# Kernel tuning notes

Measured on AMD Instinct MI355X. Metric: run time of the kernel, lower is better.

Reference implementation:

```python
import jax, jax.numpy as jnp
import numpy as np

LATENT = 512
RNN = 512
CODE = 512
INP = 2
MIX = 5
BATCH = 4096
SEGMENTS = 512


def _p(key, shape, scale=0.05):
    return jax.random.normal(key, shape, dtype=jnp.float32) * scale


def setup_inputs() -> dict:
    key = jax.random.key(0)
    ks = jax.random.split(key, 20)
    return {
        "latent": jax.random.normal(ks[0], (BATCH, LATENT), dtype=jnp.float32),
        "W_unpack": _p(ks[1], (CODE, LATENT)),
        "b_unpack": _p(ks[2], (CODE,)),
        "W_ih1": _p(ks[3], (4 * RNN, CODE + INP)),
        "W_hh1": _p(ks[4], (4 * RNN, RNN)),
        "b_ih1": _p(ks[5], (4 * RNN,)),
        "b_hh1": _p(ks[6], (4 * RNN,)),
        "W_ih2": _p(ks[7], (4 * RNN, RNN)),
        "W_hh2": _p(ks[8], (4 * RNN, RNN)),
        "b_ih2": _p(ks[9], (4 * RNN,)),
        "b_hh2": _p(ks[10], (4 * RNN,)),
        "W_mu": _p(ks[11], (MIX, RNN)),
        "b_mu": _p(ks[12], (MIX,)),
        "W_var": _p(ks[13], (MIX, RNN)),
        "b_var": _p(ks[14], (MIX,)),
        "W_mix": _p(ks[15], (MIX, RNN)),
        "b_mix": _p(ks[16], (MIX,)),
        "eps": jax.random.normal(ks[17], (SEGMENTS, BATCH, 1), dtype=jnp.float32),
        "num_segments": SEGMENTS,
    }


def _lstm_cell(x, h, c, W_ih, W_hh, b_ih, b_hh):
    # PyTorch LSTMCell: gate order i, f, g, o
    gates = x @ W_ih.T + b_ih + h @ W_hh.T + b_hh
    i, f, g, o = jnp.split(gates, 4, axis=-1)
    c_new = jax.nn.sigmoid(f) * c + jax.nn.sigmoid(i) * jnp.tanh(g)
    h_new = jax.nn.sigmoid(o) * jnp.tanh(c_new)
    return h_new, c_new


def reference(latent, W_unpack, b_unpack, W_ih1, W_hh1, b_ih1, b_hh1,
              W_ih2, W_hh2, b_ih2, b_hh2, W_mu, b_mu, W_var, b_var,
              W_mix, b_mix, eps, num_segments):
    t = 0.0  # default temperature arg
    B = latent.shape[0]
    idea = jnp.tanh(latent @ W_unpack.T + b_unpack)  # [B, CODE]

    def step(carry, eps_s):
        prev, h1, c1, h2, c2 = carry
        x = jnp.concatenate([idea, prev], axis=-1)          # [B, CODE+2]
        h1, c1 = _lstm_cell(x, h1, c1, W_ih1, W_hh1, b_ih1, b_hh1)
        h2, c2 = _lstm_cell(h1, h2, c2, W_ih2, W_hh2, b_ih2, b_hh2)
        rho = jax.nn.softmax(h2 @ W_mix.T + b_mix, axis=-1)  # [B, MIX]
        mu = jnp.sum(rho * (h2 @ W_mu.T + b_mu), axis=-1, keepdims=True)
        sigma = jnp.sum(rho * jnp.exp(h2 @ W_var.T + b_var - t), axis=-1, keepdims=True)
        angles = jnp.tanh(mu + sigma * eps_s)                # rsample + tanh, [B, 1]
        prev = jnp.concatenate([angles, jnp.zeros_like(angles)], axis=-1)
        return (prev, h1, c1, h2, c2), angles

    z = jnp.zeros((B, RNN), dtype=latent.dtype)
    carry0 = (jnp.zeros((B, INP), dtype=latent.dtype), z, z, z, z)
    _, angles = jax.lax.scan(step, carry0, eps)              # [S, B, 1]
    level = jnp.concatenate([angles, jnp.zeros_like(angles)], axis=-1)  # [S, B, 2]
    return jnp.transpose(level, (1, 0, 2))                   # [B, S, 2]
```

## Files before the change

kernel.cpp:

```cpp
#include <hip/hip_runtime.h>
#include <stdint.h>

#define BATCH 4096
#define RNN   512
#define SEGS  512

typedef __attribute__((ext_vector_type(8))) short bf16x8;
typedef __attribute__((ext_vector_type(4))) float f32x4;

#define MODE_TANH  0
#define MODE_BASE  1
#define MODE_CELL1 2
#define MODE_CELL2 3

#define GLD_LDS16(g, l) \
  __builtin_amdgcn_global_load_lds((const __attribute__((address_space(1))) void*)(g), \
                                   (__attribute__((address_space(3))) void*)(l), 16, 0, 0)

__device__ __forceinline__ unsigned short f2bf(float f){
  unsigned u = __float_as_uint(f);
  u += 0x7FFF + ((u >> 16) & 1);
  return (unsigned short)(u >> 16);
}
__device__ __forceinline__ float bf2f(unsigned short s){
  return __uint_as_float(((unsigned)s) << 16);
}
__device__ __forceinline__ float fsigmoid(float x){ return 1.0f / (1.0f + __expf(-x)); }
__device__ __forceinline__ float ftanh(float x){
  float e = __expf(-2.0f * fabsf(x));
  float t = (1.0f - e) / (1.0f + e);
  return copysignf(t, x);
}


__global__ void prep_cvt(const float* __restrict__ x, short* __restrict__ y, int n){
  int i = blockIdx.x * 256 + threadIdx.x;
  if (i < n) y[i] = (short)f2bf(x[i]);
}

__global__ void prep_reorder(
    const float* __restrict__ W_ih1, const float* __restrict__ W_hh1,
    const float* __restrict__ b_ih1, const float* __restrict__ b_hh1,
    const float* __restrict__ W_ih2, const float* __restrict__ W_hh2,
    const float* __restrict__ b_ih2, const float* __restrict__ b_hh2,
    short* __restrict__ Wr1, short* __restrict__ W1c,
    short* __restrict__ Wr2i, short* __restrict__ Wr2h,
    float* __restrict__ w1r, float* __restrict__ b1r, float* __restrict__ b2r)
{
  int idx = blockIdx.x * 256 + threadIdx.x;
  if (idx >= 2048 * 512) return;
  int rn = idx >> 9;
  int k  = idx & 511;
  int j = rn >> 2, g = rn & 3;
  int ro = g * 512 + j;
  Wr1 [idx] = (short)f2bf(W_hh1[(size_t)ro * 512 + k]);
  W1c [idx] = (short)f2bf(W_ih1[(size_t)ro * 514 + k]);
  Wr2i[idx] = (short)f2bf(W_ih2[(size_t)ro * 512 + k]);
  Wr2h[idx] = (short)f2bf(W_hh2[(size_t)ro * 512 + k]);
  if (k == 0){
    w1r[rn] = W_ih1[(size_t)ro * 514 + 512];
    b1r[rn] = b_ih1[ro] + b_hh1[ro];
    b2r[rn] = b_ih2[ro] + b_hh2[ro];
  }
}

__global__ void prep_whead(const float* __restrict__ Wmu, const float* __restrict__ Wvar,
                           const float* __restrict__ Wmix, short* __restrict__ Wh){
  int i = blockIdx.x * 256 + threadIdx.x;
  if (i >= 16 * 512) return;
  int n = i >> 9, k = i & 511;
  float v = (n < 5) ? Wmu[n * 512 + k] : (n < 10) ? Wvar[(n - 5) * 512 + k]
          : (n < 15) ? Wmix[(n - 10) * 512 + k] : 0.f;
  Wh[i] = (short)f2bf(v);
}

__global__ __launch_bounds__(256) void gemm_fused(
    const short* __restrict__ A1, const short* __restrict__ B1,
    const short* __restrict__ A2, const short* __restrict__ B2,
    int k1, int k2, int N, int mode,
    const float* __restrict__ bias,
    const unsigned short* __restrict__ base1,
    const float* __restrict__ w1r,
    float* __restrict__ cbuf,
    void* __restrict__ outp,
    const short* __restrict__ h2prev, const short* __restrict__ Whead,
    const float* __restrict__ bmu, const float* __restrict__ bvar,
    const float* __restrict__ bmix, const float* __restrict__ eps,
    float* __restrict__ fout, int s)
{
  __shared__ __align__(16) short As[8192];
  __shared__ __align__(16) short Bs[8192];
  __shared__ __align__(16) float headP[128 * 16];
  __shared__ float angS[128];

  const int tid  = threadIdx.x;
  const int lane = tid & 63;
  const int wave = tid >> 6;
  const int wm = wave >> 1, wn = wave & 1;
  const int m0 = blockIdx.y * 128, n0 = blockIdx.x * 128;

  int aoff[4], boff[4];
  #pragma unroll
  for (int j = 0; j < 4; j++){
    int c = (wave * 4 + j) * 64 + lane;
    int quad = c & 3, r16 = (c >> 2) & 15, kw = (c >> 6) & 1, g = c >> 7;
    int row = g * 16 + r16, col = kw * 32 + quad * 8;
    aoff[j] = (m0 + row) * 512 + col;
    boff[j] = (n0 + row) * 512 + col;
  }

  f32x4 acc[4][4];
  #pragma unroll
  for (int i = 0; i < 4; i++)
    #pragma unroll
    for (int j = 0; j < 4; j++)
      acc[i][j] = (f32x4){0.f, 0.f, 0.f, 0.f};

  const int nk = (k1 + k2) >> 6;

  auto stage = [&](int it){
    int ko = it << 6;
    const short* Ap; const short* Bp; int kk;
    if (ko < k1){ Ap = A1; Bp = B1; kk = ko; }
    else        { Ap = A2; Bp = B2; kk = ko - k1; }
    #pragma unroll
    for (int j = 0; j < 4; j++){
      GLD_LDS16(Ap + aoff[j] + kk, (char*)As + (wave * 4 + j) * 1024);
      GLD_LDS16(Bp + boff[j] + kk, (char*)Bs + (wave * 4 + j) * 1024);
    }
  };

  const int fro = ((lane & 15) * 4 + (lane >> 4)) * 8;

  auto compute = [&](){
    #pragma unroll
    for (int kw = 0; kw < 2; ++kw){
      bf16x8 af[4], bfr[4];
      #pragma unroll
      for (int f = 0; f < 4; f++){
        af[f]  = *(const bf16x8*)&As[((wm * 4 + f) * 2 + kw) * 512 + fro];
        bfr[f] = *(const bf16x8*)&Bs[((wn * 4 + f) * 2 + kw) * 512 + fro];
      }
      #pragma unroll
      for (int mf = 0; mf < 4; mf++)
        #pragma unroll
        for (int nf = 0; nf < 4; nf++)
          acc[mf][nf] = __builtin_amdgcn_mfma_f32_16x16x32_bf16(af[mf], bfr[nf], acc[mf][nf], 0, 0, 0);
    }
  };

  stage(0);

  if (mode == MODE_CELL1 && s > 0){
    const int g0 = wave * 2;
    f32x4 pa0 = {0.f,0.f,0.f,0.f}, pa1 = {0.f,0.f,0.f,0.f};
    const int arow = m0 + g0 * 16 + (lane & 15);
    const int koff = (lane >> 4) * 8;
    #pragma unroll
    for (int k0 = 0; k0 < 512; k0 += 32){
      bf16x8 bfh = *(const bf16x8*)&Whead[(lane & 15) * 512 + k0 + koff];
      bf16x8 a0  = *(const bf16x8*)&h2prev[(size_t)arow * 512 + k0 + koff];
      bf16x8 a1  = *(const bf16x8*)&h2prev[(size_t)(arow + 16) * 512 + k0 + koff];
      pa0 = __builtin_amdgcn_mfma_f32_16x16x32_bf16(a0, bfh, pa0, 0, 0, 0);
      pa1 = __builtin_amdgcn_mfma_f32_16x16x32_bf16(a1, bfh, pa1, 0, 0, 0);
    }
    #pragma unroll
    for (int r = 0; r < 4; r++){
      headP[((g0    ) * 16 + (lane >> 4) * 4 + r) * 16 + (lane & 15)] = pa0[r];
      headP[((g0 + 1) * 16 + (lane >> 4) * 4 + r) * 16 + (lane & 15)] = pa1[r];
    }
  }

  __syncthreads();

  if (mode == MODE_CELL1){
    if (s > 0){
      if (tid < 128){
        float p[15];
        #pragma unroll
        for (int k = 0; k < 15; k++) p[k] = headP[tid * 16 + k];
        float l[5], mx = -1e30f;
        #pragma unroll
        for (int k = 0; k < 5; k++){ l[k] = p[10 + k] + bmix[k]; mx = fmaxf(mx, l[k]); }
        float se = 0.f, e[5];
        #pragma unroll
        for (int k = 0; k < 5; k++){ e[k] = __expf(l[k] - mx); se += e[k]; }
        float inv = 1.0f / se, mu = 0.f, sg = 0.f;
        #pragma unroll
        for (int k = 0; k < 5; k++){
          float rho = e[k] * inv;
          mu += rho * (p[k] + bmu[k]);
          sg += rho * __expf(p[5 + k] + bvar[k]);
        }
        float a = ftanh(mu + sg * eps[(size_t)(s - 1) * BATCH + m0 + tid]);
        angS[tid] = a;
        if (blockIdx.x == 0){
          size_t o = ((size_t)(m0 + tid) * SEGS + (s - 1)) * 2;
          fout[o] = a; fout[o + 1] = 0.0f;
        }
      }
    } else if (tid < 128) angS[tid] = 0.f;
  }

  compute();
  __syncthreads();

  for (int it = 1; it < nk; ++it){
    stage(it);
    __syncthreads();
    compute();
    __syncthreads();
  }

  const int lr = (lane >> 4) * 4;
  const int lc = lane & 15;

  if (mode == MODE_TANH){
    unsigned short* out = (unsigned short*)outp;
    #pragma unroll
    for (int mf = 0; mf < 4; mf++)
      #pragma unroll
      for (int nf = 0; nf < 4; nf++)
        #pragma unroll
        for (int r = 0; r < 4; r++){
          int grow = m0 + wm * 64 + mf * 16 + lr + r;
          int gcol = n0 + wn * 64 + nf * 16 + lc;
          float v = acc[mf][nf][r] + bias[gcol];
          out[(size_t)grow * N + gcol] = f2bf(ftanh(v));
        }
  } else if (mode == MODE_BASE){
    unsigned short* out = (unsigned short*)outp;
    #pragma unroll
    for (int mf = 0; mf < 4; mf++)
      #pragma unroll
      for (int nf = 0; nf < 4; nf++)
        #pragma unroll
        for (int r = 0; r < 4; r++){
          int grow = m0 + wm * 64 + mf * 16 + lr + r;
          int gcol = n0 + wn * 64 + nf * 16 + lc;
          out[(size_t)grow * N + gcol] = f2bf(acc[mf][nf][r] + bias[gcol]);
        }
  } else {
    unsigned short* hout = (unsigned short*)outp;
    const int q = lane & 3;
    #pragma unroll
    for (int mf = 0; mf < 4; mf++)
      #pragma unroll
      for (int nf = 0; nf < 4; nf++)
        #pragma unroll
        for (int r = 0; r < 4; r++){
          int grow = m0 + wm * 64 + mf * 16 + lr + r;
          int gcol = n0 + wn * 64 + nf * 16 + lc;
          float v = acc[mf][nf][r];
          if (mode == MODE_CELL1)
            v += bf2f(base1[(size_t)grow * 2048 + gcol]) + angS[grow - m0] * w1r[gcol];
          else
            v += bias[gcol];
          float x1 = __shfl_xor(v, 1);
          float x2 = __shfl_xor(v, 2);
          float x3 = __shfl_xor(v, 3);
          if (q == 0){
            int j = gcol >> 2;
            size_t ci = (size_t)grow * 512 + j;
            float co = cbuf[ci];
            float cn = fsigmoid(x1) * co + fsigmoid(v) * ftanh(x2);
            float hn = fsigmoid(x3) * ftanh(cn);
            cbuf[ci] = cn;
            hout[ci] = f2bf(hn);
          }
        }
  }
}

__global__ __launch_bounds__(256) void head_step(
    const short* __restrict__ h2,
    const float* __restrict__ Wmu,  const float* __restrict__ bmu,
    const float* __restrict__ Wvar, const float* __restrict__ bvar,
    const float* __restrict__ Wmix, const float* __restrict__ bmix,
    const float* __restrict__ eps,  float* __restrict__ ang,
    float* __restrict__ out, int s)
{
  const int lane = threadIdx.x & 63;
  const int wave = threadIdx.x >> 6;
  const int row = blockIdx.x * 4 + wave;

  uint4 hv = *(const uint4*)&h2[(size_t)row * 512 + lane * 8];
  const unsigned short* hs = (const unsigned short*)&hv;
  float h[8];
  #pragma unroll
  for (int j = 0; j < 8; j++) h[j] = bf2f(hs[j]);

  float p[15];
  #pragma unroll
  for (int k = 0; k < 5; k++){
    const float4* wm4 = (const float4*)(Wmu  + (size_t)k * 512 + lane * 8);
    const float4* wv4 = (const float4*)(Wvar + (size_t)k * 512 + lane * 8);
    const float4* wx4 = (const float4*)(Wmix + (size_t)k * 512 + lane * 8);
    float4 a0 = wm4[0], a1 = wm4[1];
    float4 v0 = wv4[0], v1 = wv4[1];
    float4 x0 = wx4[0], x1 = wx4[1];
    p[k]      = h[0]*a0.x + h[1]*a0.y + h[2]*a0.z + h[3]*a0.w + h[4]*a1.x + h[5]*a1.y + h[6]*a1.z + h[7]*a1.w;
    p[5 + k]  = h[0]*v0.x + h[1]*v0.y + h[2]*v0.z + h[3]*v0.w + h[4]*v1.x + h[5]*v1.y + h[6]*v1.z + h[7]*v1.w;
    p[10 + k] = h[0]*x0.x + h[1]*x0.y + h[2]*x0.z + h[3]*x0.w + h[4]*x1.x + h[5]*x1.y + h[6]*x1.z + h[7]*x1.w;
  }
  #pragma unroll
  for (int k = 0; k < 15; k++){
    #pragma unroll
    for (int off = 1; off < 64; off <<= 1)
      p[k] += __shfl_xor(p[k], off);
  }
  if (lane == 0){
    float l[5], mx = -1e30f;
    #pragma unroll
    for (int k = 0; k < 5; k++){ l[k] = p[10 + k] + bmix[k]; mx = fmaxf(mx, l[k]); }
    float se = 0.f, e[5];
    #pragma unroll
    for (int k = 0; k < 5; k++){ e[k] = __expf(l[k] - mx); se += e[k]; }
    float inv = 1.0f / se, mu = 0.f, sg = 0.f;
    #pragma unroll
    for (int k = 0; k < 5; k++){
      float rho = e[k] * inv;
      mu += rho * (p[k] + bmu[k]);
      sg += rho * __expf(p[5 + k] + bvar[k]);
    }
    float a = ftanh(mu + sg * eps[(size_t)s * BATCH + row]);
    ang[row] = a;
    size_t o = ((size_t)row * SEGS + s) * 2;
    out[o]     = a;
    out[o + 1] = 0.0f;
  }
}


extern "C" void kernel_launch(void* const* d_in, const int* in_sizes, int n_in,
                              void* d_out, int out_size, void* d_ws, size_t ws_size,
                              hipStream_t stream)
{
  const float* latent   = (const float*)d_in[0];
  const float* W_unpack = (const float*)d_in[1];
  const float* b_unpack = (const float*)d_in[2];
  const float* W_ih1    = (const float*)d_in[3];
  const float* W_hh1    = (const float*)d_in[4];
  const float* b_ih1    = (const float*)d_in[5];
  const float* b_hh1    = (const float*)d_in[6];
  const float* W_ih2    = (const float*)d_in[7];
  const float* W_hh2    = (const float*)d_in[8];
  const float* b_ih2    = (const float*)d_in[9];
  const float* b_hh2    = (const float*)d_in[10];
  const float* W_mu     = (const float*)d_in[11];
  const float* b_mu     = (const float*)d_in[12];
  const float* W_var    = (const float*)d_in[13];
  const float* b_var    = (const float*)d_in[14];
  const float* W_mix    = (const float*)d_in[15];
  const float* b_mix    = (const float*)d_in[16];
  const float* eps      = (const float*)d_in[17];
  float* out = (float*)d_out;

  char* p = (char*)d_ws;
  auto alloc = [&](size_t b) -> void* {
    void* r = (void*)p;
    p += (b + 255) & ~(size_t)255;
    return r;
  };
  short* latb  = (short*)alloc((size_t)BATCH * 512 * 2);
  short* Wub   = (short*)alloc((size_t)512 * 512 * 2);
  short* idea  = (short*)alloc((size_t)BATCH * 512 * 2);
  unsigned short* base1 = (unsigned short*)alloc((size_t)BATCH * 2048 * 2);
  short* Wr1   = (short*)alloc((size_t)2048 * 512 * 2);
  short* W1c   = (short*)alloc((size_t)2048 * 512 * 2);
  short* Wr2i  = (short*)alloc((size_t)2048 * 512 * 2);
  short* Wr2h  = (short*)alloc((size_t)2048 * 512 * 2);
  short* Whead = (short*)alloc((size_t)16 * 512 * 2);
  float* w1r   = (float*)alloc(2048 * 4);
  float* b1r   = (float*)alloc(2048 * 4);
  float* b2r   = (float*)alloc(2048 * 4);
  short* h1a   = (short*)alloc((size_t)BATCH * 512 * 2);
  short* h1b   = (short*)alloc((size_t)BATCH * 512 * 2);
  short* h2a   = (short*)alloc((size_t)BATCH * 512 * 2);
  short* h2b   = (short*)alloc((size_t)BATCH * 512 * 2);
  float* c1    = (float*)alloc((size_t)BATCH * 512 * 4);
  float* c2    = (float*)alloc((size_t)BATCH * 512 * 4);
  float* ang   = (float*)alloc(BATCH * 4);
  short* h1[2] = {h1a, h1b};
  short* h2[2] = {h2a, h2b};

  hipMemsetAsync(h1[0], 0, (size_t)BATCH * 512 * 2, stream);
  hipMemsetAsync(h2[0], 0, (size_t)BATCH * 512 * 2, stream);
  hipMemsetAsync(c1, 0, (size_t)BATCH * 512 * 4, stream);
  hipMemsetAsync(c2, 0, (size_t)BATCH * 512 * 4, stream);

  prep_cvt<<<(BATCH * 512) / 256, 256, 0, stream>>>(latent, latb, BATCH * 512);
  prep_cvt<<<(512 * 512) / 256, 256, 0, stream>>>(W_unpack, Wub, 512 * 512);
  prep_reorder<<<(2048 * 512) / 256, 256, 0, stream>>>(
      W_ih1, W_hh1, b_ih1, b_hh1, W_ih2, W_hh2, b_ih2, b_hh2,
      Wr1, W1c, Wr2i, Wr2h, w1r, b1r, b2r);
  prep_whead<<<32, 256, 0, stream>>>(W_mu, W_var, W_mix, Whead);

  dim3 blk(256);
  gemm_fused<<<dim3(4, 32), blk, 0, stream>>>(
      latb, Wub, nullptr, nullptr, 512, 0, 512, MODE_TANH,
      b_unpack, nullptr, nullptr, nullptr, (void*)idea,
      nullptr, nullptr, nullptr, nullptr, nullptr, nullptr, nullptr, 0);
  gemm_fused<<<dim3(16, 32), blk, 0, stream>>>(
      idea, W1c, nullptr, nullptr, 512, 0, 2048, MODE_BASE,
      b1r, nullptr, nullptr, nullptr, (void*)base1,
      nullptr, nullptr, nullptr, nullptr, nullptr, nullptr, nullptr, 0);

  int cur = 0;
  for (int s = 0; s < SEGS; ++s){
    gemm_fused<<<dim3(16, 32), blk, 0, stream>>>(
        h1[cur], Wr1, nullptr, nullptr, 512, 0, 2048, MODE_CELL1,
        nullptr, base1, w1r, c1, (void*)h1[cur ^ 1],
        h2[cur], Whead, b_mu, b_var, b_mix, eps, out, s);
    gemm_fused<<<dim3(16, 32), blk, 0, stream>>>(
        h1[cur ^ 1], Wr2i, h2[cur], Wr2h, 512, 512, 2048, MODE_CELL2,
        b2r, nullptr, nullptr, c2, (void*)h2[cur ^ 1],
        nullptr, nullptr, nullptr, nullptr, nullptr, nullptr, nullptr, 0);
    cur ^= 1;
  }
  head_step<<<BATCH / 4, 256, 0, stream>>>(
      h2[cur], W_mu, b_mu, W_var, b_var, W_mix, b_mix, eps, ang, out, SEGS - 1);
}
```

Baseline: 61.10 ms.

## Replace per-step kernel launches with a persistent grid-synchronized LSTM scan kernel

Moves the 512-step recurrence from 1024 separate kernel launches into one persistent kernel that loops over steps and tiles. Phases are separated by an atomic-counter grid barrier, with the grid size taken from the occupancy query. This removes launch overhead and the gaps between dependent launches, at the cost of spin-wait barrier latency. The barrier relies on all blocks being co-resident and has a timeout bail-out that could silently break ordering.

```diff
diff --git a/kernel.cpp b/kernel.cpp
--- a/kernel.cpp
+++ b/kernel.cpp
@@ -90,8 +90,6 @@
 {
   __shared__ __align__(16) short As[8192];
   __shared__ __align__(16) short Bs[8192];
-  __shared__ __align__(16) float headP[128 * 16];
-  __shared__ float angS[128];
 
   const int tid  = threadIdx.x;
   const int lane = tid & 63;
@@ -150,8 +148,140 @@
   };
 
   stage(0);
-
-  if (mode == MODE_CELL1 && s > 0){
+  __syncthreads();
+  compute();
+  __syncthreads();
+  for (int it = 1; it < nk; ++it){
+    stage(it);
+    __syncthreads();
+    compute();
+    __syncthreads();
+  }
+
+  const int lr = (lane >> 4) * 4;
+  const int lc = lane & 15;
+
+  if (mode == MODE_TANH){
+    unsigned short* out = (unsigned short*)outp;
+    #pragma unroll
+    for (int mf = 0; mf < 4; mf++)
+      #pragma unroll
+      for (int nf = 0; nf < 4; nf++)
+        #pragma unroll
+        for (int r = 0; r < 4; r++){
+          int grow = m0 + wm * 64 + mf * 16 + lr + r;
+          int gcol = n0 + wn * 64 + nf * 16 + lc;
+          float v = acc[mf][nf][r] + bias[gcol];
+          out[(size_t)grow * N + gcol] = f2bf(ftanh(v));
+        }
+  } else {
+    unsigned short* out = (unsigned short*)outp;
+    #pragma unroll
+    for (int mf = 0; mf < 4; mf++)
+      #pragma unroll
+      for (int nf = 0; nf < 4; nf++)
+        #pragma unroll
+        for (int r = 0; r < 4; r++){
+          int grow = m0 + wm * 64 + mf * 16 + lr + r;
+          int gcol = n0 + wn * 64 + nf * 16 + lc;
+          out[(size_t)grow * N + gcol] = f2bf(acc[mf][nf][r] + bias[gcol]);
+        }
+  }
+}
+
+__device__ __forceinline__ void gridbar(unsigned* cnt, int G, int& gen, bool& bail){
+  __syncthreads();
+  if (threadIdx.x == 0){
+    gen++;
+    __threadfence();
+    __hip_atomic_fetch_add(cnt, 1u, __ATOMIC_RELAXED, __HIP_MEMORY_SCOPE_AGENT);
+    if (!bail){
+      const unsigned tgt = (unsigned)G * (unsigned)gen;
+      unsigned iters = 0;
+      while (__hip_atomic_load(cnt, __ATOMIC_RELAXED, __HIP_MEMORY_SCOPE_AGENT) < tgt){
+        __builtin_amdgcn_s_sleep(2);
+        if (++iters > (1u << 24)) { bail = true; break; }
+      }
+    }
+    __threadfence();
+  }
+  __syncthreads();
+}
+
+template<int PHASE>
+__device__ __forceinline__ void run_tile(
+    int t, int s,
+    const short* __restrict__ A1, const short* __restrict__ B1,
+    const short* __restrict__ A2, const short* __restrict__ B2,
+    const unsigned short* __restrict__ base1, const float* __restrict__ w1r,
+    const float* __restrict__ bias2,
+    float* __restrict__ cbuf, unsigned short* __restrict__ hout,
+    const short* __restrict__ h2prev, const short* __restrict__ Whead,
+    const float* __restrict__ bmu, const float* __restrict__ bvar,
+    const float* __restrict__ bmix, const float* __restrict__ eps,
+    float* __restrict__ fout,
+    short* As, short* Bs, float* headP, float* angS)
+{
+  const int tid  = threadIdx.x;
+  const int lane = tid & 63;
+  const int wave = tid >> 6;
+  const int wm = wave >> 1, wn = wave & 1;
+  const int bx = t & 15, by = t >> 4;
+  const int m0 = by * 128, n0 = bx * 128;
+
+  int aoff[4], boff[4];
+  #pragma unroll
+  for (int j = 0; j < 4; j++){
+    int c = (wave * 4 + j) * 64 + lane;
+    int quad = c & 3, r16 = (c >> 2) & 15, kw = (c >> 6) & 1, g = c >> 7;
+    int row = g * 16 + r16, col = kw * 32 + quad * 8;
+    aoff[j] = (m0 + row) * 512 + col;
+    boff[j] = (n0 + row) * 512 + col;
+  }
+
+  f32x4 acc[4][4];
+  #pragma unroll
+  for (int i = 0; i < 4; i++)
+    #pragma unroll
+    for (int j = 0; j < 4; j++)
+      acc[i][j] = (f32x4){0.f, 0.f, 0.f, 0.f};
+
+  const int nk = (PHASE == 1) ? 8 : 16;
+
+  auto stage = [&](int it){
+    int ko = it << 6;
+    const short* Ap; const short* Bp; int kk;
+    if (PHASE == 1 || ko < 512){ Ap = A1; Bp = B1; kk = ko; }
+    else                       { Ap = A2; Bp = B2; kk = ko - 512; }
+    #pragma unroll
+    for (int j = 0; j < 4; j++){
+      GLD_LDS16(Ap + aoff[j] + kk, (char*)As + (wave * 4 + j) * 1024);
+      GLD_LDS16(Bp + boff[j] + kk, (char*)Bs + (wave * 4 + j) * 1024);
+    }
+  };
+
+  const int fro = ((lane & 15) * 4 + (lane >> 4)) * 8;
+
+  auto compute = [&](){
+    #pragma unroll
+    for (int kw = 0; kw < 2; ++kw){
+      bf16x8 af[4], bfr[4];
+      #pragma unroll
+      for (int f = 0; f < 4; f++){
+        af[f]  = *(const bf16x8*)&As[((wm * 4 + f) * 2 + kw) * 512 + fro];
+        bfr[f] = *(const bf16x8*)&Bs[((wn * 4 + f) * 2 + kw) * 512 + fro];
+      }
+      #pragma unroll
+      for (int mf = 0; mf < 4; mf++)
+        #pragma unroll
+        for (int nf = 0; nf < 4; nf++)
+          acc[mf][nf] = __builtin_amdgcn_mfma_f32_16x16x32_bf16(af[mf], bfr[nf], acc[mf][nf], 0, 0, 0);
+    }
+  };
+
+  stage(0);
+
+  if (PHASE == 1 && s > 0){
     const int g0 = wave * 2;
     f32x4 pa0 = {0.f,0.f,0.f,0.f}, pa1 = {0.f,0.f,0.f,0.f};
     const int arow = m0 + g0 * 16 + (lane & 15);
@@ -173,7 +303,7 @@
 
   __syncthreads();
 
-  if (mode == MODE_CELL1){
+  if (PHASE == 1){
     if (s > 0){
       if (tid < 128){
         float p[15];
@@ -194,7 +324,7 @@
         }
         float a = ftanh(mu + sg * eps[(size_t)(s - 1) * BATCH + m0 + tid]);
         angS[tid] = a;
-        if (blockIdx.x == 0){
+        if (bx == 0){
           size_t o = ((size_t)(m0 + tid) * SEGS + (s - 1)) * 2;
           fout[o] = a; fout[o + 1] = 0.0f;
         }
@@ -214,61 +344,74 @@
 
   const int lr = (lane >> 4) * 4;
   const int lc = lane & 15;
-
-  if (mode == MODE_TANH){
-    unsigned short* out = (unsigned short*)outp;
-    #pragma unroll
-    for (int mf = 0; mf < 4; mf++)
-      #pragma unroll
-      for (int nf = 0; nf < 4; nf++)
-        #pragma unroll
-        for (int r = 0; r < 4; r++){
-          int grow = m0 + wm * 64 + mf * 16 + lr + r;
-          int gcol = n0 + wn * 64 + nf * 16 + lc;
-          float v = acc[mf][nf][r] + bias[gcol];
-          out[(size_t)grow * N + gcol] = f2bf(ftanh(v));
+  const int q = lane & 3;
+  #pragma unroll
+  for (int mf = 0; mf < 4; mf++)
+    #pragma unroll
+    for (int nf = 0; nf < 4; nf++)
+      #pragma unroll
+      for (int r = 0; r < 4; r++){
+        int grow = m0 + wm * 64 + mf * 16 + lr + r;
+        int gcol = n0 + wn * 64 + nf * 16 + lc;
+        float v = acc[mf][nf][r];
+        if (PHASE == 1)
+          v += bf2f(base1[(size_t)grow * 2048 + gcol]) + angS[grow - m0] * w1r[gcol];
+        else
+          v += bias2[gcol];
+        float x1 = __shfl_xor(v, 1);
+        float x2 = __shfl_xor(v, 2);
+        float x3 = __shfl_xor(v, 3);
+        if (q == 0){
+          int j = gcol >> 2;
+          size_t ci = (size_t)grow * 512 + j;
+          float co = cbuf[ci];
+          float cn = fsigmoid(x1) * co + fsigmoid(v) * ftanh(x2);
+          float hn = fsigmoid(x3) * ftanh(cn);
+          cbuf[ci] = cn;
+          hout[ci] = f2bf(hn);
         }
-  } else if (mode == MODE_BASE){
-    unsigned short* out = (unsigned short*)outp;
-    #pragma unroll
-    for (int mf = 0; mf < 4; mf++)
-      #pragma unroll
-      for (int nf = 0; nf < 4; nf++)
-        #pragma unroll
-        for (int r = 0; r < 4; r++){
-          int grow = m0 + wm * 64 + mf * 16 + lr + r;
-          int gcol = n0 + wn * 64 + nf * 16 + lc;
-          out[(size_t)grow * N + gcol] = f2bf(acc[mf][nf][r] + bias[gcol]);
-        }
-  } else {
-    unsigned short* hout = (unsigned short*)outp;
-    const int q = lane & 3;
-    #pragma unroll
-    for (int mf = 0; mf < 4; mf++)
-      #pragma unroll
-      for (int nf = 0; nf < 4; nf++)
-        #pragma unroll
-        for (int r = 0; r < 4; r++){
-          int grow = m0 + wm * 64 + mf * 16 + lr + r;
-          int gcol = n0 + wn * 64 + nf * 16 + lc;
-          float v = acc[mf][nf][r];
-          if (mode == MODE_CELL1)
-            v += bf2f(base1[(size_t)grow * 2048 + gcol]) + angS[grow - m0] * w1r[gcol];
-          else
-            v += bias[gcol];
-          float x1 = __shfl_xor(v, 1);
-          float x2 = __shfl_xor(v, 2);
-          float x3 = __shfl_xor(v, 3);
-          if (q == 0){
-            int j = gcol >> 2;
-            size_t ci = (size_t)grow * 512 + j;
-            float co = cbuf[ci];
-            float cn = fsigmoid(x1) * co + fsigmoid(v) * ftanh(x2);
-            float hn = fsigmoid(x3) * ftanh(cn);
-            cbuf[ci] = cn;
-            hout[ci] = f2bf(hn);
-          }
-        }
+      }
+}
+
+__global__ __launch_bounds__(256) void lstm_scan(
+    const short* __restrict__ Wr1, const short* __restrict__ Wr2i, const short* __restrict__ Wr2h,
+    const unsigned short* __restrict__ base1,
+    const float* __restrict__ w1r, const float* __restrict__ b2r,
+    float* __restrict__ c1, float* __restrict__ c2,
+    short* __restrict__ h1A, short* __restrict__ h1B,
+    short* __restrict__ h2A, short* __restrict__ h2B,
+    const short* __restrict__ Whead,
+    const float* __restrict__ bmu, const float* __restrict__ bvar, const float* __restrict__ bmix,
+    const float* __restrict__ eps, float* __restrict__ fout,
+    unsigned* __restrict__ barcnt)
+{
+  __shared__ __align__(16) short As[8192];
+  __shared__ __align__(16) short Bs[8192];
+  __shared__ __align__(16) float headP[128 * 16];
+  __shared__ float angS[128];
+
+  const int bid = blockIdx.x;
+  const int G   = gridDim.x;
+  int gen = 0;
+  bool bail = false;
+
+  for (int s = 0; s < SEGS; ++s){
+    const short* h1in  = (s & 1) ? h1B : h1A;
+    short*       h1out = (s & 1) ? h1A : h1B;
+    const short* h2in  = (s & 1) ? h2B : h2A;
+    short*       h2out = (s & 1) ? h2A : h2B;
+
+    for (int t = bid; t < 512; t += G)
+      run_tile<1>(t, s, h1in, Wr1, nullptr, nullptr, base1, w1r, nullptr,
+                  c1, (unsigned short*)h1out, h2in, Whead, bmu, bvar, bmix,
+                  eps, fout, As, Bs, headP, angS);
+    gridbar(barcnt, G, gen, bail);
+
+    for (int t = bid; t < 512; t += G)
+      run_tile<2>(t, s, h1out, Wr2i, h2in, Wr2h, nullptr, nullptr, b2r,
+                  c2, (unsigned short*)h2out, nullptr, nullptr, nullptr, nullptr,
+                  nullptr, nullptr, fout, As, Bs, headP, angS);
+    gridbar(barcnt, G, gen, bail);
   }
 }
 
@@ -381,13 +524,26 @@
   float* c1    = (float*)alloc((size_t)BATCH * 512 * 4);
   float* c2    = (float*)alloc((size_t)BATCH * 512 * 4);
   float* ang   = (float*)alloc(BATCH * 4);
-  short* h1[2] = {h1a, h1b};
-  short* h2[2] = {h2a, h2b};
-
-  hipMemsetAsync(h1[0], 0, (size_t)BATCH * 512 * 2, stream);
-  hipMemsetAsync(h2[0], 0, (size_t)BATCH * 512 * 2, stream);
+  unsigned* barcnt = (unsigned*)alloc(256);
+
+  static int g_G = 0;
+  if (g_G == 0){
+    int occ = 0, ncu = 256, dev = 0;
+    if (hipOccupancyMaxActiveBlocksPerMultiprocessor(&occ, lstm_scan, 256, 0) != hipSuccess || occ < 1)
+      occ = 1;
+    hipDeviceProp_t prop;
+    if (hipGetDevice(&dev) == hipSuccess && hipGetDeviceProperties(&prop, dev) == hipSuccess)
+      ncu = prop.multiProcessorCount;
+    long g = (long)occ * (long)ncu;
+    g_G = (g > 512) ? 512 : (int)g;
+    if (g_G < 1) g_G = 256;
+  }
+
+  hipMemsetAsync(h1a, 0, (size_t)BATCH * 512 * 2, stream);
+  hipMemsetAsync(h2a, 0, (size_t)BATCH * 512 * 2, stream);
   hipMemsetAsync(c1, 0, (size_t)BATCH * 512 * 4, stream);
   hipMemsetAsync(c2, 0, (size_t)BATCH * 512 * 4, stream);
+  hipMemsetAsync(barcnt, 0, 256, stream);
 
   prep_cvt<<<(BATCH * 512) / 256, 256, 0, stream>>>(latent, latb, BATCH * 512);
   prep_cvt<<<(512 * 512) / 256, 256, 0, stream>>>(W_unpack, Wub, 512 * 512);
@@ -406,18 +562,10 @@
       b1r, nullptr, nullptr, nullptr, (void*)base1,
       nullptr, nullptr, nullptr, nullptr, nullptr, nullptr, nullptr, 0);
 
-  int cur = 0;
-  for (int s = 0; s < SEGS; ++s){
-    gemm_fused<<<dim3(16, 32), blk, 0, stream>>>(
-        h1[cur], Wr1, nullptr, nullptr, 512, 0, 2048, MODE_CELL1,
-        nullptr, base1, w1r, c1, (void*)h1[cur ^ 1],
-        h2[cur], Whead, b_mu, b_var, b_mix, eps, out, s);
-    gemm_fused<<<dim3(16, 32), blk, 0, stream>>>(
-        h1[cur ^ 1], Wr2i, h2[cur], Wr2h, 512, 512, 2048, MODE_CELL2,
-        b2r, nullptr, nullptr, c2, (void*)h2[cur ^ 1],
-        nullptr, nullptr, nullptr, nullptr, nullptr, nullptr, nullptr, 0);
-    cur ^= 1;
-  }
+  lstm_scan<<<g_G, blk, 0, stream>>>(
+      Wr1, Wr2i, Wr2h, base1, w1r, b2r, c1, c2,
+      h1a, h1b, h2a, h2b, Whead, b_mu, b_var, b_mix, eps, out, barcnt);
+
   head_step<<<BATCH / 4, 256, 0, stream>>>(
-      h2[cur], W_mu, b_mu, W_var, b_var, W_mix, b_mix, eps, ang, out, SEGS - 1);
-}
+      h2a, W_mu, b_mu, W_var, b_var, W_mix, b_mix, eps, ang, out, SEGS - 1);
+}
```

Result: slower. 106.0 ms (+73.5%).

## Replace per-step GEMM launches with a persistent LSTM kernel holding state on-chip

Applied to the files above, without the earlier changes.

The 1024 per-timestep GEMM launches are replaced by one persistent kernel: 256 blocks, each owning 16 batch rows and looping over all 512 segments. h1/h2 live in swizzled LDS, the c states stay in registers, and the mixture head is computed in-block each step. Block-local barriers replace kernel boundaries, removing launch overhead and the global round trips for h and c. The cost is that each block streams the full recurrent weight matrices from L2/MALL every step with only 16 rows of reuse, so weight traffic grows a lot. It also runs just one 512-thread block per CU.

```diff
diff --git a/kernel.cpp b/kernel.cpp
--- a/kernel.cpp
+++ b/kernel.cpp
@@ -10,8 +10,6 @@
 
 #define MODE_TANH  0
 #define MODE_BASE  1
-#define MODE_CELL1 2
-#define MODE_CELL2 3
 
 #define GLD_LDS16(g, l) \
   __builtin_amdgcn_global_load_lds((const __attribute__((address_space(1))) void*)(g), \
@@ -76,22 +74,12 @@
 
 __global__ __launch_bounds__(256) void gemm_fused(
     const short* __restrict__ A1, const short* __restrict__ B1,
-    const short* __restrict__ A2, const short* __restrict__ B2,
-    int k1, int k2, int N, int mode,
+    int k1, int N, int mode,
     const float* __restrict__ bias,
-    const unsigned short* __restrict__ base1,
-    const float* __restrict__ w1r,
-    float* __restrict__ cbuf,
-    void* __restrict__ outp,
-    const short* __restrict__ h2prev, const short* __restrict__ Whead,
-    const float* __restrict__ bmu, const float* __restrict__ bvar,
-    const float* __restrict__ bmix, const float* __restrict__ eps,
-    float* __restrict__ fout, int s)
+    void* __restrict__ outp)
 {
   __shared__ __align__(16) short As[8192];
   __shared__ __align__(16) short Bs[8192];
-  __shared__ __align__(16) float headP[128 * 16];
-  __shared__ float angS[128];
 
   const int tid  = threadIdx.x;
   const int lane = tid & 63;
@@ -116,17 +104,14 @@
     for (int j = 0; j < 4; j++)
       acc[i][j] = (f32x4){0.f, 0.f, 0.f, 0.f};
 
-  const int nk = (k1 + k2) >> 6;
+  const int nk = k1 >> 6;
 
   auto stage = [&](int it){
-    int ko = it << 6;
-    const short* Ap; const short* Bp; int kk;
-    if (ko < k1){ Ap = A1; Bp = B1; kk = ko; }
-    else        { Ap = A2; Bp = B2; kk = ko - k1; }
+    int kk = it << 6;
     #pragma unroll
     for (int j = 0; j < 4; j++){
-      GLD_LDS16(Ap + aoff[j] + kk, (char*)As + (wave * 4 + j) * 1024);
-      GLD_LDS16(Bp + boff[j] + kk, (char*)Bs + (wave * 4 + j) * 1024);
+      GLD_LDS16(A1 + aoff[j] + kk, (char*)As + (wave * 4 + j) * 1024);
+      GLD_LDS16(B1 + boff[j] + kk, (char*)Bs + (wave * 4 + j) * 1024);
     }
   };
 
@@ -150,61 +135,9 @@
   };
 
   stage(0);
-
-  if (mode == MODE_CELL1 && s > 0){
-    const int g0 = wave * 2;
-    f32x4 pa0 = {0.f,0.f,0.f,0.f}, pa1 = {0.f,0.f,0.f,0.f};
-    const int arow = m0 + g0 * 16 + (lane & 15);
-    const int koff = (lane >> 4) * 8;
-    #pragma unroll
-    for (int k0 = 0; k0 < 512; k0 += 32){
-      bf16x8 bfh = *(const bf16x8*)&Whead[(lane & 15) * 512 + k0 + koff];
-      bf16x8 a0  = *(const bf16x8*)&h2prev[(size_t)arow * 512 + k0 + koff];
-      bf16x8 a1  = *(const bf16x8*)&h2prev[(size_t)(arow + 16) * 512 + k0 + koff];
-      pa0 = __builtin_amdgcn_mfma_f32_16x16x32_bf16(a0, bfh, pa0, 0, 0, 0);
-      pa1 = __builtin_amdgcn_mfma_f32_16x16x32_bf16(a1, bfh, pa1, 0, 0, 0);
-    }
-    #pragma unroll
-    for (int r = 0; r < 4; r++){
-      headP[((g0    ) * 16 + (lane >> 4) * 4 + r) * 16 + (lane & 15)] = pa0[r];
-      headP[((g0 + 1) * 16 + (lane >> 4) * 4 + r) * 16 + (lane & 15)] = pa1[r];
-    }
-  }
-
   __syncthreads();
-
-  if (mode == MODE_CELL1){
-    if (s > 0){
-      if (tid < 128){
-        float p[15];
-        #pragma unroll
-        for (int k = 0; k < 15; k++) p[k] = headP[tid * 16 + k];
-        float l[5], mx = -1e30f;
-        #pragma unroll
-        for (int k = 0; k < 5; k++){ l[k] = p[10 + k] + bmix[k]; mx = fmaxf(mx, l[k]); }
-        float se = 0.f, e[5];
-        #pragma unroll
-        for (int k = 0; k < 5; k++){ e[k] = __expf(l[k] - mx); se += e[k]; }
-        float inv = 1.0f / se, mu = 0.f, sg = 0.f;
-        #pragma unroll
-        for (int k = 0; k < 5; k++){
-          float rho = e[k] * inv;
-          mu += rho * (p[k] + bmu[k]);
-          sg += rho * __expf(p[5 + k] + bvar[k]);
-        }
-        float a = ftanh(mu + sg * eps[(size_t)(s - 1) * BATCH + m0 + tid]);
-        angS[tid] = a;
-        if (blockIdx.x == 0){
-          size_t o = ((size_t)(m0 + tid) * SEGS + (s - 1)) * 2;
-          fout[o] = a; fout[o + 1] = 0.0f;
-        }
-      }
-    } else if (tid < 128) angS[tid] = 0.f;
-  }
-
   compute();
   __syncthreads();
-
   for (int it = 1; it < nk; ++it){
     stage(it);
     __syncthreads();
@@ -214,120 +147,197 @@
 
   const int lr = (lane >> 4) * 4;
   const int lc = lane & 15;
-
-  if (mode == MODE_TANH){
-    unsigned short* out = (unsigned short*)outp;
-    #pragma unroll
-    for (int mf = 0; mf < 4; mf++)
-      #pragma unroll
-      for (int nf = 0; nf < 4; nf++)
-        #pragma unroll
-        for (int r = 0; r < 4; r++){
-          int grow = m0 + wm * 64 + mf * 16 + lr + r;
-          int gcol = n0 + wn * 64 + nf * 16 + lc;
-          float v = acc[mf][nf][r] + bias[gcol];
-          out[(size_t)grow * N + gcol] = f2bf(ftanh(v));
+  unsigned short* out = (unsigned short*)outp;
+  #pragma unroll
+  for (int mf = 0; mf < 4; mf++)
+    #pragma unroll
+    for (int nf = 0; nf < 4; nf++)
+      #pragma unroll
+      for (int r = 0; r < 4; r++){
+        int grow = m0 + wm * 64 + mf * 16 + lr + r;
+        int gcol = n0 + wn * 64 + nf * 16 + lc;
+        float v = acc[mf][nf][r] + bias[gcol];
+        out[(size_t)grow * N + gcol] = f2bf(mode == MODE_TANH ? ftanh(v) : v);
+      }
+}
+
+__global__ __launch_bounds__(512) void lstm_block(
+    const short* __restrict__ Wr1, const short* __restrict__ Wr2i, const short* __restrict__ Wr2h,
+    const unsigned short* __restrict__ base1,
+    const float* __restrict__ w1r, const float* __restrict__ b2r,
+    const short* __restrict__ Whead,
+    const float* __restrict__ bmu, const float* __restrict__ bvar, const float* __restrict__ bmix,
+    const float* __restrict__ eps, float* __restrict__ fout)
+{
+  __shared__ __align__(16) short hs[4][8192];
+  __shared__ float P[16 * 16];
+  __shared__ float angS[16];
+
+  const int tid  = threadIdx.x;
+  const int lane = tid & 63;
+  const int wave = tid >> 6;
+  const int r0   = blockIdx.x * 16;
+  const int lc   = lane & 15;
+  const int lr   = (lane >> 4) * 4;
+  const int q    = lane & 3;
+  const int t4   = (lane >> 2) & 3;
+  const int koff = (lane >> 4) * 8;
+  const int arow = lane & 15;
+
+  for (int i = tid; i < 4 * 8192; i += 512) ((short*)hs)[i] = 0;
+  if (tid < 16) angS[tid] = 0.f;
+  float c1r[16], c2r[16];
+  #pragma unroll
+  for (int i = 0; i < 16; i++){ c1r[i] = 0.f; c2r[i] = 0.f; }
+  __syncthreads();
+
+  auto ldA = [&](const short* h, int k0) -> bf16x8 {
+    int a = (arow << 10) | ((k0 + koff) << 1);
+    a ^= (arow & 7) << 4;
+    return *(const bf16x8*)((const char*)h + a);
+  };
+
+  for (int s = 0; s < SEGS; ++s){
+    const short* h1i = hs[s & 1];
+    short*       h1o = hs[(s & 1) ^ 1];
+    const short* h2i = hs[2 + (s & 1)];
+    short*       h2o = hs[2 + ((s & 1) ^ 1)];
+
+    #pragma unroll
+    for (int ch = 0; ch < 2; ++ch){
+      const int cb = wave * 256 + ch * 128;
+      f32x4 acc[8];
+      #pragma unroll
+      for (int nf = 0; nf < 8; ++nf) acc[nf] = (f32x4){0.f, 0.f, 0.f, 0.f};
+      const size_t bb = (size_t)(cb + lc) * 512 + koff;
+      #pragma unroll 4
+      for (int k0 = 0; k0 < 512; k0 += 32){
+        bf16x8 a = ldA(h1i, k0);
+        #pragma unroll
+        for (int nf = 0; nf < 8; ++nf){
+          bf16x8 b = *(const bf16x8*)&Wr1[bb + (size_t)nf * 8192 + k0];
+          acc[nf] = __builtin_amdgcn_mfma_f32_16x16x32_bf16(a, b, acc[nf], 0, 0, 0);
         }
-  } else if (mode == MODE_BASE){
-    unsigned short* out = (unsigned short*)outp;
-    #pragma unroll
-    for (int mf = 0; mf < 4; mf++)
-      #pragma unroll
-      for (int nf = 0; nf < 4; nf++)
-        #pragma unroll
-        for (int r = 0; r < 4; r++){
-          int grow = m0 + wm * 64 + mf * 16 + lr + r;
-          int gcol = n0 + wn * 64 + nf * 16 + lc;
-          out[(size_t)grow * N + gcol] = f2bf(acc[mf][nf][r] + bias[gcol]);
-        }
-  } else {
-    unsigned short* hout = (unsigned short*)outp;
-    const int q = lane & 3;
-    #pragma unroll
-    for (int mf = 0; mf < 4; mf++)
-      #pragma unroll
-      for (int nf = 0; nf < 4; nf++)
-        #pragma unroll
-        for (int r = 0; r < 4; r++){
-          int grow = m0 + wm * 64 + mf * 16 + lr + r;
-          int gcol = n0 + wn * 64 + nf * 16 + lc;
-          float v = acc[mf][nf][r];
-          if (mode == MODE_CELL1)
-            v += bf2f(base1[(size_t)grow * 2048 + gcol]) + angS[grow - m0] * w1r[gcol];
-          else
-            v += bias[gcol];
+      }
+      #pragma unroll
+      for (int nf = 0; nf < 8; ++nf){
+        const int gcol = cb + nf * 16 + lc;
+        const float w1 = w1r[gcol];
+        float vq = 0.f, x1q = 0.f, x2q = 0.f, x3q = 0.f;
+        #pragma unroll
+        for (int r = 0; r < 4; ++r){
+          float v = acc[nf][r] + bf2f(base1[(size_t)(r0 + lr + r) * 2048 + gcol])
+                  + angS[lr + r] * w1;
           float x1 = __shfl_xor(v, 1);
           float x2 = __shfl_xor(v, 2);
           float x3 = __shfl_xor(v, 3);
-          if (q == 0){
-            int j = gcol >> 2;
-            size_t ci = (size_t)grow * 512 + j;
-            float co = cbuf[ci];
-            float cn = fsigmoid(x1) * co + fsigmoid(v) * ftanh(x2);
-            float hn = fsigmoid(x3) * ftanh(cn);
-            cbuf[ci] = cn;
-            hout[ci] = f2bf(hn);
-          }
+          if (r == q){ vq = v; x1q = x1; x2q = x2; x3q = x3; }
         }
-  }
-}
-
-__global__ __launch_bounds__(256) void head_step(
-    const short* __restrict__ h2,
-    const float* __restrict__ Wmu,  const float* __restrict__ bmu,
-    const float* __restrict__ Wvar, const float* __restrict__ bvar,
-    const float* __restrict__ Wmix, const float* __restrict__ bmix,
-    const float* __restrict__ eps,  float* __restrict__ ang,
-    float* __restrict__ out, int s)
-{
-  const int lane = threadIdx.x & 63;
-  const int wave = threadIdx.x >> 6;
-  const int row = blockIdx.x * 4 + wave;
-
-  uint4 hv = *(const uint4*)&h2[(size_t)row * 512 + lane * 8];
-  const unsigned short* hs = (const unsigned short*)&hv;
-  float h[8];
-  #pragma unroll
-  for (int j = 0; j < 8; j++) h[j] = bf2f(hs[j]);
-
-  float p[15];
-  #pragma unroll
-  for (int k = 0; k < 5; k++){
-    const float4* wm4 = (const float4*)(Wmu  + (size_t)k * 512 + lane * 8);
-    const float4* wv4 = (const float4*)(Wvar + (size_t)k * 512 + lane * 8);
-    const float4* wx4 = (const float4*)(Wmix + (size_t)k * 512 + lane * 8);
-    float4 a0 = wm4[0], a1 = wm4[1];
-    float4 v0 = wv4[0], v1 = wv4[1];
-    float4 x0 = wx4[0], x1 = wx4[1];
-    p[k]      = h[0]*a0.x + h[1]*a0.y + h[2]*a0.z + h[3]*a0.w + h[4]*a1.x + h[5]*a1.y + h[6]*a1.z + h[7]*a1.w;
-    p[5 + k]  = h[0]*v0.x + h[1]*v0.y + h[2]*v0.z + h[3]*v0.w + h[4]*v1.x + h[5]*v1.y + h[6]*v1.z + h[7]*v1.w;
-    p[10 + k] = h[0]*x0.x + h[1]*x0.y + h[2]*x0.z + h[3]*x0.w + h[4]*x1.x + h[5]*x1.y + h[6]*x1.z + h[7]*x1.w;
-  }
-  #pragma unroll
-  for (int k = 0; k < 15; k++){
-    #pragma unroll
-    for (int off = 1; off < 64; off <<= 1)
-      p[k] += __shfl_xor(p[k], off);
-  }
-  if (lane == 0){
-    float l[5], mx = -1e30f;
-    #pragma unroll
-    for (int k = 0; k < 5; k++){ l[k] = p[10 + k] + bmix[k]; mx = fmaxf(mx, l[k]); }
-    float se = 0.f, e[5];
-    #pragma unroll
-    for (int k = 0; k < 5; k++){ e[k] = __expf(l[k] - mx); se += e[k]; }
-    float inv = 1.0f / se, mu = 0.f, sg = 0.f;
-    #pragma unroll
-    for (int k = 0; k < 5; k++){
-      float rho = e[k] * inv;
-      mu += rho * (p[k] + bmu[k]);
-      sg += rho * __expf(p[5 + k] + bvar[k]);
-    }
-    float a = ftanh(mu + sg * eps[(size_t)s * BATCH + row]);
-    ang[row] = a;
-    size_t o = ((size_t)row * SEGS + s) * 2;
-    out[o]     = a;
-    out[o + 1] = 0.0f;
+        float gi = (q == 0) ? vq  : (q == 1) ? x1q : (q == 2) ? x2q : x3q;
+        float gf = (q == 0) ? x1q : (q == 1) ? vq  : (q == 2) ? x3q : x2q;
+        float gg = (q == 0) ? x2q : (q == 1) ? x3q : (q == 2) ? vq  : x1q;
+        float go = (q == 0) ? x3q : (q == 1) ? x2q : (q == 2) ? x1q : vq;
+        const int ci = ch * 8 + nf;
+        float cn = fsigmoid(gf) * c1r[ci] + fsigmoid(gi) * ftanh(gg);
+        float hn = fsigmoid(go) * ftanh(cn);
+        c1r[ci] = cn;
+        const int row = lr + q;
+        const int j   = ((cb + nf * 16) >> 2) + t4;
+        int wb = ((row << 10) | (j << 1)) ^ ((row & 7) << 4);
+        *(unsigned short*)((char*)h1o + wb) = f2bf(hn);
+      }
+    }
+    __syncthreads();
+
+    #pragma unroll
+    for (int ch = 0; ch < 2; ++ch){
+      const int cb = wave * 256 + ch * 128;
+      f32x4 acc[8];
+      #pragma unroll
+      for (int nf = 0; nf < 8; ++nf) acc[nf] = (f32x4){0.f, 0.f, 0.f, 0.f};
+      const size_t bb = (size_t)(cb + lc) * 512 + koff;
+      #pragma unroll 4
+      for (int k0 = 0; k0 < 512; k0 += 32){
+        bf16x8 a = ldA(h1o, k0);
+        #pragma unroll
+        for (int nf = 0; nf < 8; ++nf){
+          bf16x8 b = *(const bf16x8*)&Wr2i[bb + (size_t)nf * 8192 + k0];
+          acc[nf] = __builtin_amdgcn_mfma_f32_16x16x32_bf16(a, b, acc[nf], 0, 0, 0);
+        }
+      }
+      #pragma unroll 4
+      for (int k0 = 0; k0 < 512; k0 += 32){
+        bf16x8 a = ldA(h2i, k0);
+        #pragma unroll
+        for (int nf = 0; nf < 8; ++nf){
+          bf16x8 b = *(const bf16x8*)&Wr2h[bb + (size_t)nf * 8192 + k0];
+          acc[nf] = __builtin_amdgcn_mfma_f32_16x16x32_bf16(a, b, acc[nf], 0, 0, 0);
+        }
+      }
+      #pragma unroll
+      for (int nf = 0; nf < 8; ++nf){
+        const int gcol = cb + nf * 16 + lc;
+        float vq = 0.f, x1q = 0.f, x2q = 0.f, x3q = 0.f;
+        #pragma unroll
+        for (int r = 0; r < 4; ++r){
+          float v = acc[nf][r] + b2r[gcol];
+          float x1 = __shfl_xor(v, 1);
+          float x2 = __shfl_xor(v, 2);
+          float x3 = __shfl_xor(v, 3);
+          if (r == q){ vq = v; x1q = x1; x2q = x2; x3q = x3; }
+        }
+        float gi = (q == 0) ? vq  : (q == 1) ? x1q : (q == 2) ? x2q : x3q;
+        float gf = (q == 0) ? x1q : (q == 1) ? vq  : (q == 2) ? x3q : x2q;
+        float gg = (q == 0) ? x2q : (q == 1) ? x3q : (q == 2) ? vq  : x1q;
+        float go = (q == 0) ? x3q : (q == 1) ? x2q : (q == 2) ? x1q : vq;
+        const int ci = ch * 8 + nf;
+        float cn = fsigmoid(gf) * c2r[ci] + fsigmoid(gi) * ftanh(gg);
+        float hn = fsigmoid(go) * ftanh(cn);
+        c2r[ci] = cn;
+        const int row = lr + q;
+        const int j   = ((cb + nf * 16) >> 2) + t4;
+        int wb = ((row << 10) | (j << 1)) ^ ((row & 7) << 4);
+        *(unsigned short*)((char*)h2o + wb) = f2bf(hn);
+      }
+    }
+    __syncthreads();
+
+    if (wave == 0){
+      f32x4 pa = (f32x4){0.f, 0.f, 0.f, 0.f};
+      #pragma unroll 4
+      for (int k0 = 0; k0 < 512; k0 += 32){
+        bf16x8 a = ldA(h2o, k0);
+        bf16x8 b = *(const bf16x8*)&Whead[(size_t)lc * 512 + k0 + koff];
+        pa = __builtin_amdgcn_mfma_f32_16x16x32_bf16(a, b, pa, 0, 0, 0);
+      }
+      #pragma unroll
+      for (int r = 0; r < 4; ++r) P[(lr + r) * 16 + lc] = pa[r];
+    }
+    __syncthreads();
+
+    if (wave == 0 && lane < 16){
+      float p[15];
+      #pragma unroll
+      for (int k = 0; k < 15; k++) p[k] = P[lane * 16 + k];
+      float l[5], mx = -1e30f;
+      #pragma unroll
+      for (int k = 0; k < 5; k++){ l[k] = p[10 + k] + bmix[k]; mx = fmaxf(mx, l[k]); }
+      float se = 0.f, e[5];
+      #pragma unroll
+      for (int k = 0; k < 5; k++){ e[k] = __expf(l[k] - mx); se += e[k]; }
+      float inv = 1.0f / se, mu = 0.f, sg = 0.f;
+      #pragma unroll
+      for (int k = 0; k < 5; k++){
+        float rho = e[k] * inv;
+        mu += rho * (p[k] + bmu[k]);
+        sg += rho * __expf(p[5 + k] + bvar[k]);
+      }
+      float a = ftanh(mu + sg * eps[(size_t)s * BATCH + r0 + lane]);
+      angS[lane] = a;
+      size_t o = ((size_t)(r0 + lane) * SEGS + s) * 2;
+      fout[o] = a; fout[o + 1] = 0.0f;
+    }
+    __syncthreads();
   }
 }
 
@@ -374,20 +384,6 @@
   float* w1r   = (float*)alloc(2048 * 4);
   float* b1r   = (float*)alloc(2048 * 4);
   float* b2r   = (float*)alloc(2048 * 4);
-  short* h1a   = (short*)alloc((size_t)BATCH * 512 * 2);
-  short* h1b   = (short*)alloc((size_t)BATCH * 512 * 2);
-  short* h2a   = (short*)alloc((size_t)BATCH * 512 * 2);
-  short* h2b   = (short*)alloc((size_t)BATCH * 512 * 2);
-  float* c1    = (float*)alloc((size_t)BATCH * 512 * 4);
-  float* c2    = (float*)alloc((size_t)BATCH * 512 * 4);
-  float* ang   = (float*)alloc(BATCH * 4);
-  short* h1[2] = {h1a, h1b};
-  short* h2[2] = {h2a, h2b};
-
-  hipMemsetAsync(h1[0], 0, (size_t)BATCH * 512 * 2, stream);
-  hipMemsetAsync(h2[0], 0, (size_t)BATCH * 512 * 2, stream);
-  hipMemsetAsync(c1, 0, (size_t)BATCH * 512 * 4, stream);
-  hipMemsetAsync(c2, 0, (size_t)BATCH * 512 * 4, stream);
 
   prep_cvt<<<(BATCH * 512) / 256, 256, 0, stream>>>(latent, latb, BATCH * 512);
   prep_cvt<<<(512 * 512) / 256, 256, 0, stream>>>(W_unpack, Wub, 512 * 512);
@@ -398,26 +394,11 @@
 
   dim3 blk(256);
   gemm_fused<<<dim3(4, 32), blk, 0, stream>>>(
-      latb, Wub, nullptr, nullptr, 512, 0, 512, MODE_TANH,
-      b_unpack, nullptr, nullptr, nullptr, (void*)idea,
-      nullptr, nullptr, nullptr, nullptr, nullptr, nullptr, nullptr, 0);
+      latb, Wub, 512, 512, MODE_TANH, b_unpack, (void*)idea);
   gemm_fused<<<dim3(16, 32), blk, 0, stream>>>(
-      idea, W1c, nullptr, nullptr, 512, 0, 2048, MODE_BASE,
-      b1r, nullptr, nullptr, nullptr, (void*)base1,
-      nullptr, nullptr, nullptr, nullptr, nullptr, nullptr, nullptr, 0);
-
-  int cur = 0;
-  for (int s = 0; s < SEGS; ++s){
-    gemm_fused<<<dim3(16, 32), blk, 0, stream>>>(
-        h1[cur], Wr1, nullptr, nullptr, 512, 0, 2048, MODE_CELL1,
-        nullptr, base1, w1r, c1, (void*)h1[cur ^ 1],
-        h2[cur], Whead, b_mu, b_var, b_mix, eps, out, s);
-    gemm_fused<<<dim3(16, 32), blk, 0, stream>>>(
-        h1[cur ^ 1], Wr2i, h2[cur], Wr2h, 512, 512, 2048, MODE_CELL2,
-        b2r, nullptr, nullptr, c2, (void*)h2[cur ^ 1],
-        nullptr, nullptr, nullptr, nullptr, nullptr, nullptr, nullptr, 0);
-    cur ^= 1;
-  }
-  head_step<<<BATCH / 4, 256, 0, stream>>>(
-      h2[cur], W_mu, b_mu, W_var, b_var, W_mix, b_mix, eps, ang, out, SEGS - 1);
-}
+      idea, W1c, 512, 2048, MODE_BASE, b1r, (void*)base1);
+
+  lstm_block<<<256, 512, 0, stream>>>(
+      Wr1, Wr2i, Wr2h, base1, w1r, b2r, Whead,
+      b_mu, b_var, b_mix, eps, out);
+}
```

Measured after the change: 113.1 ms. 1.85x slower.
